# Kernel tuning notes

Hardware: AMD Instinct MI355X
Metric: run time of the kernel (lower is better)

Reference implementation:

```python
import jax, jax.numpy as jnp
import numpy as np

N = 500_000      # total nodes across all graphs in batch
B = 128          # batch_size (number of graphs)
S = 128          # state_size
D = 128          # aggregated_size


def setup_inputs() -> dict:
    key = jax.random.key(0)
    k1, k2, k3, k4, k5, k6 = jax.random.split(key, 6)
    nodes = jax.random.normal(k1, (N, S), dtype=jnp.float32)
    owner_masks = jax.random.randint(k2, (B, N), 0, 2, dtype=jnp.int32)
    # Linear params (torch Linear: y = x @ W.T + b); store W as [in, out] for x @ W
    scale = 1.0 / np.sqrt(S)
    Wt = jax.random.uniform(k3, (S, D), jnp.float32, -scale, scale)
    bt = jax.random.uniform(k4, (D,), jnp.float32, -scale, scale)
    Wg = jax.random.uniform(k5, (S, D), jnp.float32, -scale, scale)
    bg = jax.random.uniform(k6, (D,), jnp.float32, -scale, scale)
    return {"nodes": nodes, "owner_masks": owner_masks,
            "Wt": Wt, "bt": bt, "Wg": Wg, "bg": bg}


def reference(nodes, owner_masks, Wt, bt, Wg, bg):
    # gates = sigmoid(nodes @ Wg + bg)   [N, D]
    gates = jax.nn.sigmoid(nodes @ Wg + bg)
    # data = nodes @ Wt + bt             [N, D]
    data = nodes @ Wt + bt
    # pooled = owner_masks.float() @ (data * gates)   [B, D]
    return owner_masks.astype(jnp.float32) @ (data * gates)
```

## Files before the change

kernel.cpp:

```cpp
#include <hip/hip_runtime.h>


#define NTOT   500000
#define NBLK   512
#define NCHUNK 15625

typedef __attribute__((ext_vector_type(8))) unsigned short ushort8;
typedef __bf16 bf16x8 __attribute__((ext_vector_type(8)));
typedef __bf16 bf16x2 __attribute__((ext_vector_type(2)));
typedef __attribute__((ext_vector_type(4))) float f32x4;

static __device__ __forceinline__ unsigned int pkbf(float a, float b) {
  bf16x2 v;
  v[0] = (__bf16)a;
  v[1] = (__bf16)b;
  return __builtin_bit_cast(unsigned int, v);
}

static __device__ __forceinline__ unsigned int mkw(int lo, int hi) {
  return (lo ? 0x3F80u : 0u) | (hi ? 0x3F800000u : 0u);
}

template <bool ATOMIC>
__global__ __launch_bounds__(256, 2)
void agg_main(const float* __restrict__ nodes, const int* __restrict__ masks,
              const float* __restrict__ Wt, const float* __restrict__ bt,
              const float* __restrict__ Wg, const float* __restrict__ bg,
              float* __restrict__ outp) {
  __shared__ __align__(16) unsigned short nodes_s[2][32][136];
  __shared__ __align__(16) unsigned short vt_s[2][128][40];

  const int tid = threadIdx.x;
  const int lane = tid & 63;
  const int w = tid >> 6;
  const int q = lane >> 4;
  const int r = lane & 15;

  bf16x8 Wf[2][4][2];
  float btr[2], bgr[2];
#pragma unroll
  for (int nt = 0; nt < 2; ++nt) {
    const int d = w * 32 + nt * 16 + r;
    btr[nt] = bt[d];
    bgr[nt] = bg[d];
#pragma unroll
    for (int ks = 0; ks < 4; ++ks) {
      ushort8 ft, fg;
#pragma unroll
      for (int j = 0; j < 8; ++j) {
        const int k = ks * 32 + q * 8 + j;
        ft[j] = __builtin_bit_cast(unsigned short, (__bf16)Wt[k * 128 + d]);
        fg[j] = __builtin_bit_cast(unsigned short, (__bf16)Wg[k * 128 + d]);
      }
      Wf[0][ks][nt] = __builtin_bit_cast(bf16x8, ft);
      Wf[1][ks][nt] = __builtin_bit_cast(bf16x8, fg);
    }
  }

  f32x4 acc[2][8];
  const f32x4 fzero = {0.f, 0.f, 0.f, 0.f};
#pragma unroll
  for (int i = 0; i < 2; ++i)
#pragma unroll
    for (int j = 0; j < 8; ++j) acc[i][j] = fzero;

  const int bid = blockIdx.x;
  const int c0 = (int)(((long long)bid * NCHUNK) / NBLK);
  const int c1 = (int)(((long long)(bid + 1) * NCHUNK) / NBLK);
  const int n = c1 - c0;

  const int* mrow0 = masks + (size_t)(w * 32 + r) * NTOT + q * 8;
  const int* mrow1 = mrow0 + (size_t)16 * NTOT;

  float4 nf[4];
  int4 miA[2][2], miB[2][2];

  auto issue_nodes = [&](int c) {
    const float4* p = (const float4*)(nodes + (size_t)c * 32 * 128);
#pragma unroll
    for (int it = 0; it < 4; ++it) nf[it] = p[it * 256 + tid];
  };

  auto issue_masks = [&](int4 (&mi)[2][2], int c) {
    const int k0 = c * 32;
    mi[0][0] = *(const int4*)(mrow0 + k0);
    mi[0][1] = *(const int4*)(mrow0 + k0 + 4);
    mi[1][0] = *(const int4*)(mrow1 + k0);
    mi[1][1] = *(const int4*)(mrow1 + k0 + 4);
  };

  auto stage = [&](int buf) {
#pragma unroll
    for (int it = 0; it < 4; ++it) {
      const int flat = it * 256 + tid;
      const int nrow = flat >> 5, nc4 = flat & 31;
      uint2 u;
      u.x = pkbf(nf[it].x, nf[it].y);
      u.y = pkbf(nf[it].z, nf[it].w);
      *(uint2*)&nodes_s[buf][nrow][nc4 * 4] = u;
    }
  };

  auto pool = [&](const int4 (&mi)[2][2], int buf) {
    uint4 u0, u1;
    u0.x = mkw(mi[0][0].x, mi[0][0].y);
    u0.y = mkw(mi[0][0].z, mi[0][0].w);
    u0.z = mkw(mi[0][1].x, mi[0][1].y);
    u0.w = mkw(mi[0][1].z, mi[0][1].w);
    u1.x = mkw(mi[1][0].x, mi[1][0].y);
    u1.y = mkw(mi[1][0].z, mi[1][0].w);
    u1.z = mkw(mi[1][1].x, mi[1][1].y);
    u1.w = mkw(mi[1][1].z, mi[1][1].w);
    const bf16x8 af0 = __builtin_bit_cast(bf16x8, u0);
    const bf16x8 af1 = __builtin_bit_cast(bf16x8, u1);
#pragma unroll
    for (int nt = 0; nt < 8; ++nt) {
      const bf16x8 bfr = *(const bf16x8*)&vt_s[buf][nt * 16 + r][q * 8];
      acc[0][nt] = __builtin_amdgcn_mfma_f32_16x16x32_bf16(af0, bfr, acc[0][nt], 0, 0, 0);
      acc[1][nt] = __builtin_amdgcn_mfma_f32_16x16x32_bf16(af1, bfr, acc[1][nt], 0, 0, 0);
    }
  };

  auto gemm_epi = [&](int buf) {
    f32x4 aD[2][2], aG[2][2];
#pragma unroll
    for (int i2 = 0; i2 < 2; ++i2)
#pragma unroll
      for (int j2 = 0; j2 < 2; ++j2) { aD[i2][j2] = fzero; aG[i2][j2] = fzero; }
#pragma unroll
    for (int ks = 0; ks < 4; ++ks) {
      const bf16x8 a0 = *(const bf16x8*)&nodes_s[buf][r][ks * 32 + q * 8];
      const bf16x8 a1 = *(const bf16x8*)&nodes_s[buf][16 + r][ks * 32 + q * 8];
#pragma unroll
      for (int nt = 0; nt < 2; ++nt) {
        aD[0][nt] = __builtin_amdgcn_mfma_f32_16x16x32_bf16(a0, Wf[0][ks][nt], aD[0][nt], 0, 0, 0);
        aD[1][nt] = __builtin_amdgcn_mfma_f32_16x16x32_bf16(a1, Wf[0][ks][nt], aD[1][nt], 0, 0, 0);
        aG[0][nt] = __builtin_amdgcn_mfma_f32_16x16x32_bf16(a0, Wf[1][ks][nt], aG[0][nt], 0, 0, 0);
        aG[1][nt] = __builtin_amdgcn_mfma_f32_16x16x32_bf16(a1, Wf[1][ks][nt], aG[1][nt], 0, 0, 0);
      }
    }
#pragma unroll
    for (int mt = 0; mt < 2; ++mt)
#pragma unroll
      for (int nt = 0; nt < 2; ++nt) {
        const int d = w * 32 + nt * 16 + r;
        float v[4];
#pragma unroll
        for (int reg = 0; reg < 4; ++reg) {
          const float x = aD[mt][nt][reg] + btr[nt];
          const float g = aG[mt][nt][reg] + bgr[nt];
          v[reg] = x * __builtin_amdgcn_rcpf(1.f + __expf(-g));
        }
        uint2 u;
        u.x = pkbf(v[0], v[1]);
        u.y = pkbf(v[2], v[3]);
        *(uint2*)&vt_s[buf][d][mt * 16 + q * 4] = u;
      }
  };

  int i = 0;
  auto body = [&](int buf, int4 (&mip)[2][2], int4 (&mii)[2][2]) {
    stage(buf);
    __syncthreads();
    const int c = c0 + i;
    if (i + 1 < n) issue_nodes(c + 1);
    if (i > 0) pool(mip, buf ^ 1);
    if (i + 1 < n) issue_masks(mii, c + 1);
    gemm_epi(buf);
    ++i;
  };

  if (n > 0) {
    issue_nodes(c0);
    issue_masks(miA, c0);
  }
  while (i < n) {
    body(0, miB, miB);
    if (i < n) body(1, miA, miA);
  }
  __syncthreads();
  if (n > 0) {
    if ((n - 1) & 1) pool(miB, 1);
    else             pool(miA, 0);
  }

#pragma unroll
  for (int mt = 0; mt < 2; ++mt)
#pragma unroll
    for (int nt = 0; nt < 8; ++nt)
#pragma unroll
      for (int reg = 0; reg < 4; ++reg) {
        const int b = w * 32 + mt * 16 + q * 4 + reg;
        const int d = nt * 16 + r;
        if (ATOMIC)
          atomicAdd(&outp[b * 128 + d], acc[mt][nt][reg]);
        else
          outp[(size_t)bid * 16384 + b * 128 + d] = acc[mt][nt][reg];
      }
}

__global__ __launch_bounds__(256)
void agg_reduce(const float* __restrict__ part, float* __restrict__ out) {
  const int gid = blockIdx.x * 256 + threadIdx.x;
  const int i = gid & 16383;
  const int grp = gid >> 14;
  const float* p = part + (size_t)grp * 64 * 16384 + i;
  float s = 0.f;
#pragma unroll 8
  for (int g = 0; g < 64; ++g) s += p[(size_t)g * 16384];
  atomicAdd(&out[i], s);
}

extern "C" void kernel_launch(void* const* d_in, const int* in_sizes, int n_in,
                              void* d_out, int out_size, void* d_ws, size_t ws_size,
                              hipStream_t stream) {
  const float* nodes = (const float*)d_in[0];
  const int*   masks = (const int*)d_in[1];
  const float* Wt    = (const float*)d_in[2];
  const float* bt    = (const float*)d_in[3];
  const float* Wg    = (const float*)d_in[4];
  const float* bg    = (const float*)d_in[5];
  float* out = (float*)d_out;

  hipMemsetAsync(d_out, 0, (size_t)out_size * sizeof(float), stream);

  const size_t need = (size_t)NBLK * 16384 * sizeof(float);
  if (ws_size >= need) {
    agg_main<false><<<NBLK, 256, 0, stream>>>(nodes, masks, Wt, bt, Wg, bg, (float*)d_ws);
    agg_reduce<<<512, 256, 0, stream>>>((const float*)d_ws, out);
  } else {
    agg_main<true><<<NBLK, 256, 0, stream>>>(nodes, masks, Wt, bt, Wg, bg, out);
  }
}
```

Baseline: 526.6 us.

## Double block size to 512 threads, halving per-wave tile work

Each block now runs 8 waves instead of 4. Each wave owns 16 output columns for the gate/data GEMM and 16 graph rows for the pooling MFMA, where it previously owned 32 of each. This halves register use per thread and the per-thread load counts, and aims for more waves in flight to hide the latency of the mask and node streams. The cost is more waves competing for LDS and the barriers, plus a launch bound that asks the compiler for 4 blocks of 512 threads per CU.

```diff
diff --git a/kernel.cpp b/kernel.cpp
--- a/kernel.cpp
+++ b/kernel.cpp
@@ -22,7 +22,7 @@
 }
 
 template <bool ATOMIC>
-__global__ __launch_bounds__(256, 2)
+__global__ __launch_bounds__(512, 4)
 void agg_main(const float* __restrict__ nodes, const int* __restrict__ masks,
               const float* __restrict__ Wt, const float* __restrict__ bt,
               const float* __restrict__ Wg, const float* __restrict__ bg,
@@ -36,63 +36,54 @@
   const int q = lane >> 4;
   const int r = lane & 15;
 
-  bf16x8 Wf[2][4][2];
-  float btr[2], bgr[2];
-#pragma unroll
-  for (int nt = 0; nt < 2; ++nt) {
-    const int d = w * 32 + nt * 16 + r;
-    btr[nt] = bt[d];
-    bgr[nt] = bg[d];
-#pragma unroll
-    for (int ks = 0; ks < 4; ++ks) {
-      ushort8 ft, fg;
-#pragma unroll
-      for (int j = 0; j < 8; ++j) {
-        const int k = ks * 32 + q * 8 + j;
-        ft[j] = __builtin_bit_cast(unsigned short, (__bf16)Wt[k * 128 + d]);
-        fg[j] = __builtin_bit_cast(unsigned short, (__bf16)Wg[k * 128 + d]);
-      }
-      Wf[0][ks][nt] = __builtin_bit_cast(bf16x8, ft);
-      Wf[1][ks][nt] = __builtin_bit_cast(bf16x8, fg);
-    }
-  }
-
-  f32x4 acc[2][8];
+  bf16x8 Wf[2][4];
+  const int dslc = w * 16 + r;
+  const float btr = bt[dslc];
+  const float bgr = bg[dslc];
+#pragma unroll
+  for (int ks = 0; ks < 4; ++ks) {
+    ushort8 ft, fg;
+#pragma unroll
+    for (int j = 0; j < 8; ++j) {
+      const int k = ks * 32 + q * 8 + j;
+      ft[j] = __builtin_bit_cast(unsigned short, (__bf16)Wt[k * 128 + dslc]);
+      fg[j] = __builtin_bit_cast(unsigned short, (__bf16)Wg[k * 128 + dslc]);
+    }
+    Wf[0][ks] = __builtin_bit_cast(bf16x8, ft);
+    Wf[1][ks] = __builtin_bit_cast(bf16x8, fg);
+  }
+
+  f32x4 acc[8];
   const f32x4 fzero = {0.f, 0.f, 0.f, 0.f};
 #pragma unroll
-  for (int i = 0; i < 2; ++i)
-#pragma unroll
-    for (int j = 0; j < 8; ++j) acc[i][j] = fzero;
+  for (int j = 0; j < 8; ++j) acc[j] = fzero;
 
   const int bid = blockIdx.x;
   const int c0 = (int)(((long long)bid * NCHUNK) / NBLK);
   const int c1 = (int)(((long long)(bid + 1) * NCHUNK) / NBLK);
   const int n = c1 - c0;
 
-  const int* mrow0 = masks + (size_t)(w * 32 + r) * NTOT + q * 8;
-  const int* mrow1 = mrow0 + (size_t)16 * NTOT;
-
-  float4 nf[4];
-  int4 miA[2][2], miB[2][2];
+  const int* mrow = masks + (size_t)(w * 16 + r) * NTOT + q * 8;
+
+  float4 nf[2];
+  int4 miA[2], miB[2];
 
   auto issue_nodes = [&](int c) {
     const float4* p = (const float4*)(nodes + (size_t)c * 32 * 128);
-#pragma unroll
-    for (int it = 0; it < 4; ++it) nf[it] = p[it * 256 + tid];
-  };
-
-  auto issue_masks = [&](int4 (&mi)[2][2], int c) {
+    nf[0] = p[tid];
+    nf[1] = p[512 + tid];
+  };
+
+  auto issue_masks = [&](int4 (&mi)[2], int c) {
     const int k0 = c * 32;
-    mi[0][0] = *(const int4*)(mrow0 + k0);
-    mi[0][1] = *(const int4*)(mrow0 + k0 + 4);
-    mi[1][0] = *(const int4*)(mrow1 + k0);
-    mi[1][1] = *(const int4*)(mrow1 + k0 + 4);
+    mi[0] = *(const int4*)(mrow + k0);
+    mi[1] = *(const int4*)(mrow + k0 + 4);
   };
 
   auto stage = [&](int buf) {
 #pragma unroll
-    for (int it = 0; it < 4; ++it) {
-      const int flat = it * 256 + tid;
+    for (int it = 0; it < 2; ++it) {
+      const int flat = it * 512 + tid;
       const int nrow = flat >> 5, nc4 = flat & 31;
       uint2 u;
       u.x = pkbf(nf[it].x, nf[it].y);
@@ -101,65 +92,50 @@
     }
   };
 
-  auto pool = [&](const int4 (&mi)[2][2], int buf) {
-    uint4 u0, u1;
-    u0.x = mkw(mi[0][0].x, mi[0][0].y);
-    u0.y = mkw(mi[0][0].z, mi[0][0].w);
-    u0.z = mkw(mi[0][1].x, mi[0][1].y);
-    u0.w = mkw(mi[0][1].z, mi[0][1].w);
-    u1.x = mkw(mi[1][0].x, mi[1][0].y);
-    u1.y = mkw(mi[1][0].z, mi[1][0].w);
-    u1.z = mkw(mi[1][1].x, mi[1][1].y);
-    u1.w = mkw(mi[1][1].z, mi[1][1].w);
-    const bf16x8 af0 = __builtin_bit_cast(bf16x8, u0);
-    const bf16x8 af1 = __builtin_bit_cast(bf16x8, u1);
+  auto pool = [&](const int4 (&mi)[2], int buf) {
+    uint4 u;
+    u.x = mkw(mi[0].x, mi[0].y);
+    u.y = mkw(mi[0].z, mi[0].w);
+    u.z = mkw(mi[1].x, mi[1].y);
+    u.w = mkw(mi[1].z, mi[1].w);
+    const bf16x8 af = __builtin_bit_cast(bf16x8, u);
 #pragma unroll
     for (int nt = 0; nt < 8; ++nt) {
       const bf16x8 bfr = *(const bf16x8*)&vt_s[buf][nt * 16 + r][q * 8];
-      acc[0][nt] = __builtin_amdgcn_mfma_f32_16x16x32_bf16(af0, bfr, acc[0][nt], 0, 0, 0);
-      acc[1][nt] = __builtin_amdgcn_mfma_f32_16x16x32_bf16(af1, bfr, acc[1][nt], 0, 0, 0);
+      acc[nt] = __builtin_amdgcn_mfma_f32_16x16x32_bf16(af, bfr, acc[nt], 0, 0, 0);
     }
   };
 
   auto gemm_epi = [&](int buf) {
-    f32x4 aD[2][2], aG[2][2];
-#pragma unroll
-    for (int i2 = 0; i2 < 2; ++i2)
-#pragma unroll
-      for (int j2 = 0; j2 < 2; ++j2) { aD[i2][j2] = fzero; aG[i2][j2] = fzero; }
+    f32x4 aD[2], aG[2];
+    aD[0] = fzero; aD[1] = fzero; aG[0] = fzero; aG[1] = fzero;
 #pragma unroll
     for (int ks = 0; ks < 4; ++ks) {
       const bf16x8 a0 = *(const bf16x8*)&nodes_s[buf][r][ks * 32 + q * 8];
       const bf16x8 a1 = *(const bf16x8*)&nodes_s[buf][16 + r][ks * 32 + q * 8];
-#pragma unroll
-      for (int nt = 0; nt < 2; ++nt) {
-        aD[0][nt] = __builtin_amdgcn_mfma_f32_16x16x32_bf16(a0, Wf[0][ks][nt], aD[0][nt], 0, 0, 0);
-        aD[1][nt] = __builtin_amdgcn_mfma_f32_16x16x32_bf16(a1, Wf[0][ks][nt], aD[1][nt], 0, 0, 0);
-        aG[0][nt] = __builtin_amdgcn_mfma_f32_16x16x32_bf16(a0, Wf[1][ks][nt], aG[0][nt], 0, 0, 0);
-        aG[1][nt] = __builtin_amdgcn_mfma_f32_16x16x32_bf16(a1, Wf[1][ks][nt], aG[1][nt], 0, 0, 0);
+      aD[0] = __builtin_amdgcn_mfma_f32_16x16x32_bf16(a0, Wf[0][ks], aD[0], 0, 0, 0);
+      aD[1] = __builtin_amdgcn_mfma_f32_16x16x32_bf16(a1, Wf[0][ks], aD[1], 0, 0, 0);
+      aG[0] = __builtin_amdgcn_mfma_f32_16x16x32_bf16(a0, Wf[1][ks], aG[0], 0, 0, 0);
+      aG[1] = __builtin_amdgcn_mfma_f32_16x16x32_bf16(a1, Wf[1][ks], aG[1], 0, 0, 0);
+    }
+#pragma unroll
+    for (int mt = 0; mt < 2; ++mt) {
+      float v[4];
+#pragma unroll
+      for (int reg = 0; reg < 4; ++reg) {
+        const float x = aD[mt][reg] + btr;
+        const float g = aG[mt][reg] + bgr;
+        v[reg] = x * __builtin_amdgcn_rcpf(1.f + __expf(-g));
       }
-    }
-#pragma unroll
-    for (int mt = 0; mt < 2; ++mt)
-#pragma unroll
-      for (int nt = 0; nt < 2; ++nt) {
-        const int d = w * 32 + nt * 16 + r;
-        float v[4];
-#pragma unroll
-        for (int reg = 0; reg < 4; ++reg) {
-          const float x = aD[mt][nt][reg] + btr[nt];
-          const float g = aG[mt][nt][reg] + bgr[nt];
-          v[reg] = x * __builtin_amdgcn_rcpf(1.f + __expf(-g));
-        }
-        uint2 u;
-        u.x = pkbf(v[0], v[1]);
-        u.y = pkbf(v[2], v[3]);
-        *(uint2*)&vt_s[buf][d][mt * 16 + q * 4] = u;
-      }
+      uint2 u;
+      u.x = pkbf(v[0], v[1]);
+      u.y = pkbf(v[2], v[3]);
+      *(uint2*)&vt_s[buf][dslc][mt * 16 + q * 4] = u;
+    }
   };
 
   int i = 0;
-  auto body = [&](int buf, int4 (&mip)[2][2], int4 (&mii)[2][2]) {
+  auto body = [&](int buf, int4 (&mip)[2], int4 (&mii)[2]) {
     stage(buf);
     __syncthreads();
     const int c = c0 + i;
@@ -185,18 +161,16 @@
   }
 
 #pragma unroll
-  for (int mt = 0; mt < 2; ++mt)
-#pragma unroll
-    for (int nt = 0; nt < 8; ++nt)
-#pragma unroll
-      for (int reg = 0; reg < 4; ++reg) {
-        const int b = w * 32 + mt * 16 + q * 4 + reg;
-        const int d = nt * 16 + r;
-        if (ATOMIC)
-          atomicAdd(&outp[b * 128 + d], acc[mt][nt][reg]);
-        else
-          outp[(size_t)bid * 16384 + b * 128 + d] = acc[mt][nt][reg];
-      }
+  for (int nt = 0; nt < 8; ++nt)
+#pragma unroll
+    for (int reg = 0; reg < 4; ++reg) {
+      const int b = w * 16 + q * 4 + reg;
+      const int d = nt * 16 + r;
+      if (ATOMIC)
+        atomicAdd(&outp[b * 128 + d], acc[nt][reg]);
+      else
+        outp[(size_t)bid * 16384 + b * 128 + d] = acc[nt][reg];
+    }
 }
 
 __global__ __launch_bounds__(256)
@@ -226,9 +200,9 @@
 
   const size_t need = (size_t)NBLK * 16384 * sizeof(float);
   if (ws_size >= need) {
-    agg_main<false><<<NBLK, 256, 0, stream>>>(nodes, masks, Wt, bt, Wg, bg, (float*)d_ws);
+    agg_main<false><<<NBLK, 512, 0, stream>>>(nodes, masks, Wt, bt, Wg, bg, (float*)d_ws);
     agg_reduce<<<512, 256, 0, stream>>>((const float*)d_ws, out);
   } else {
-    agg_main<true><<<NBLK, 256, 0, stream>>>(nodes, masks, Wt, bt, Wg, bg, out);
-  }
-}
+    agg_main<true><<<NBLK, 512, 0, stream>>>(nodes, masks, Wt, bt, Wg, bg, out);
+  }
+}
```

Measured after the change: 555.7 us. +5.5%, slower.
